# Optimization experiments

Measured on AMD Instinct MI355X. Metric: run time of the kernel, lower is better.

## Reference

```python
import jax, jax.numpy as jnp
import numpy as np

D = 1024   # input_dim
H = 16     # num_heads
DH = D // H  # attention_dim per head
B, S = 4, 2048


def setup_inputs() -> dict:
    key = jax.random.key(0)
    ks = jax.random.split(key, 12)
    sc = 1.0 / np.sqrt(D)
    x = jax.random.normal(ks[0], (B, S, D), dtype=jnp.float32)
    # per-head Q/K/V linears stacked: W [H, D, DH], b [H, DH]
    Wq = jax.random.normal(ks[1], (H, D, DH), dtype=jnp.float32) * sc
    bq = jax.random.normal(ks[2], (H, DH), dtype=jnp.float32) * 0.01
    Wk = jax.random.normal(ks[3], (H, D, DH), dtype=jnp.float32) * sc
    bk = jax.random.normal(ks[4], (H, DH), dtype=jnp.float32) * 0.01
    Wv = jax.random.normal(ks[5], (H, D, DH), dtype=jnp.float32) * sc
    bv = jax.random.normal(ks[6], (H, DH), dtype=jnp.float32) * 0.01
    Wo = jax.random.normal(ks[7], (D, D), dtype=jnp.float32) * sc
    bo = jax.random.normal(ks[8], (D,), dtype=jnp.float32) * 0.01
    ln_w = jnp.ones((D,), dtype=jnp.float32)
    ln_b = jnp.zeros((D,), dtype=jnp.float32)
    return {"x": x, "Wq": Wq, "bq": bq, "Wk": Wk, "bk": bk,
            "Wv": Wv, "bv": bv, "Wo": Wo, "bo": bo,
            "ln_w": ln_w, "ln_b": ln_b}


def _layer_norm(x, w, b, eps=1e-5):
    mu = jnp.mean(x, axis=-1, keepdims=True)
    var = jnp.var(x, axis=-1, keepdims=True)
    return (x - mu) * jax.lax.rsqrt(var + eps) * w + b


def reference(x, Wq, bq, Wk, bk, Wv, bv, Wo, bo, ln_w, ln_b):
    # batched per-head projections: [B,S,D] x [H,D,DH] -> [B,H,S,DH]
    q = jnp.einsum('bsd,hde->bhse', x, Wq) + bq[None, :, None, :]
    k = jnp.einsum('bsd,hde->bhse', x, Wk) + bk[None, :, None, :]
    v = jnp.einsum('bsd,hde->bhse', x, Wv) + bv[None, :, None, :]
    scores = jnp.einsum('bhse,bhte->bhst', q, k) / np.sqrt(DH).astype(np.float32)
    weights = jax.nn.softmax(scores, axis=-1)
    attn = jnp.einsum('bhst,bhte->bhse', weights, v)          # [B,H,S,DH]
    concat = attn.transpose(0, 2, 1, 3).reshape(B, S, D)       # head-major concat
    out = concat @ Wo + bo
    return _layer_norm(x + out, ln_w, ln_b)
```

## Files before the change

kernel.cpp:

```cpp
#include <hip/hip_runtime.h>
#include <hip/hip_bf16.h>
#include <stdint.h>

constexpr int D  = 1024;
constexpr int H  = 16;
constexpr int DH = 64;
constexpr int B  = 4;
constexpr int S  = 2048;
constexpr int BS = B * S;
constexpr int NQKV = 3 * D;

typedef __attribute__((ext_vector_type(8))) short bf16x8;
typedef __attribute__((ext_vector_type(4))) float f32x4;
typedef __attribute__((ext_vector_type(16))) float f32x16;
typedef __attribute__((ext_vector_type(4))) unsigned short us4;
typedef __attribute__((ext_vector_type(4))) unsigned int u32x4;
typedef unsigned short ushort_t;

using gu32 = __attribute__((address_space(1))) unsigned int;
using lu32 = __attribute__((address_space(3))) unsigned int;

__device__ __forceinline__ void gload_lds16(const void* g, void* l) {
  __builtin_amdgcn_global_load_lds((gu32*)g, (lu32*)l, 16, 0, 0);
}

__device__ __forceinline__ ushort_t f2bf(float f) {
  uint32_t u = __builtin_bit_cast(uint32_t, f);
  u += 0x7FFFu + ((u >> 16) & 1u);
  return (ushort_t)(u >> 16);
}

__device__ __forceinline__ unsigned cvtpk(float lo, float hi) {
  unsigned r;
  asm("v_cvt_pk_bf16_f32 %0, %1, %2" : "=v"(r) : "v"(lo), "v"(hi));
  return r;
}

__device__ __forceinline__ void xch4(unsigned& w0, unsigned& w1,
                                     unsigned& w2, unsigned& w3, int hi) {
  unsigned sx = hi ? w0 : w2;
  unsigned sy = hi ? w1 : w3;
  sx = (unsigned)__shfl_xor((int)sx, 32, 64);
  sy = (unsigned)__shfl_xor((int)sy, 32, 64);
  if (hi) { w0 = sx; w1 = sy; } else { w2 = sx; w3 = sy; }
}

__global__ __launch_bounds__(256) void k_conv_x(const float* __restrict__ x,
                                                ushort_t* __restrict__ xb) {
  int i = (blockIdx.x * 256 + threadIdx.x) * 4;
  float4 v = *(const float4*)(x + i);
  us4 o;
  o[0] = f2bf(v.x); o[1] = f2bf(v.y); o[2] = f2bf(v.z); o[3] = f2bf(v.w);
  *(us4*)(xb + i) = o;
}

__global__ __launch_bounds__(256) void k_conv_w(const float* __restrict__ Wq,
                                                const float* __restrict__ Wk,
                                                const float* __restrict__ Wv,
                                                ushort_t* __restrict__ wt) {
  __shared__ ushort_t tile[64][65];
  const int bid = blockIdx.x;
  const int which = bid >> 8;
  const int hh = (bid >> 4) & 15;
  const int d0 = (bid & 15) * 64;
  const float* src = (which == 0) ? Wq : (which == 1) ? Wk : Wv;
  const int t = threadIdx.x;
  const int dd = t >> 4, e4 = (t & 15) * 4;
#pragma unroll
  for (int p = 0; p < 4; ++p) {
    int d = dd + p * 16;
    float4 v = *(const float4*)(src + ((size_t)hh * D + d0 + d) * DH + e4);
    tile[e4 + 0][d] = f2bf(v.x);
    tile[e4 + 1][d] = f2bf(v.y);
    tile[e4 + 2][d] = f2bf(v.z);
    tile[e4 + 3][d] = f2bf(v.w);
  }
  __syncthreads();
  const int e = t >> 2, dp = (t & 3) * 16;
  ushort_t* dst = wt + (size_t)(which * 1024 + hh * 64 + e) * 1024 + d0 + dp;
  us4 o[4];
#pragma unroll
  for (int g = 0; g < 4; ++g)
#pragma unroll
    for (int j = 0; j < 4; ++j) o[g][j] = tile[e][dp + g * 4 + j];
#pragma unroll
  for (int g = 0; g < 4; ++g) *(us4*)(dst + g * 4) = o[g];
}

__global__ __launch_bounds__(256) void k_conv_wo(const float* __restrict__ Wo,
                                                 ushort_t* __restrict__ wot) {
  __shared__ ushort_t tile[64][65];
  const int bid = blockIdx.x;
  const int c0 = (bid >> 4) * 64;
  const int d0 = (bid & 15) * 64;
  const int t = threadIdx.x;
  const int dd = t >> 4, e4 = (t & 15) * 4;
#pragma unroll
  for (int p = 0; p < 4; ++p) {
    int d = dd + p * 16;
    float4 v = *(const float4*)(Wo + (size_t)(d0 + d) * 1024 + c0 + e4);
    tile[e4 + 0][d] = f2bf(v.x);
    tile[e4 + 1][d] = f2bf(v.y);
    tile[e4 + 2][d] = f2bf(v.z);
    tile[e4 + 3][d] = f2bf(v.w);
  }
  __syncthreads();
  const int e = t >> 2, dp = (t & 3) * 16;
  ushort_t* dst = wot + (size_t)(c0 + e) * 1024 + d0 + dp;
  us4 o[4];
#pragma unroll
  for (int g = 0; g < 4; ++g)
#pragma unroll
    for (int j = 0; j < 4; ++j) o[g][j] = tile[e][dp + g * 4 + j];
#pragma unroll
  for (int g = 0; g < 4; ++g) *(us4*)(dst + g * 4) = o[g];
}

__device__ __forceinline__ void gemm_core_256x128(const ushort_t* __restrict__ A,
                                                  const ushort_t* __restrict__ Bt,
                                                  int m0, int n0,
                                                  f32x4 acc[4][4], char* lds) {
  const int t = threadIdx.x;
  const int lane = t & 63, w = t >> 6;
  const int wm = w >> 1, wn = w & 1;
  const int lrow = lane & 15;
  const int chx = (((lane >> 4) ^ ((lrow >> 1) & 3)) << 4);

#pragma unroll
  for (int mi = 0; mi < 4; mi++)
#pragma unroll
    for (int ni = 0; ni < 4; ni++) acc[mi][ni] = f32x4{0.f, 0.f, 0.f, 0.f};

  const int prow = t >> 2;
  const int sw16 = (((t & 3) ^ ((prow >> 1) & 3)) << 4);
  const char* sA0 = (const char*)A  + (size_t)(m0 + prow) * 2048 + sw16;
  const char* sB0 = (const char*)Bt + (size_t)(n0 + prow) * 2048 + sw16;

  auto STAGE = [&](int kt) {
    char* bb = lds + (kt % 3) * 24576;
    const size_t ko = (size_t)kt * 64;
    gload_lds16(sA0 + ko,              bb + w * 1024);
    gload_lds16(sA0 + 128 * 2048 + ko, bb + 8192 + w * 1024);
    gload_lds16(sB0 + ko,              bb + 16384 + w * 1024);
  };

  STAGE(0); STAGE(1);

  for (int kt = 0; kt < 32; ++kt) {
    if (kt < 31) asm volatile("s_waitcnt vmcnt(3)" ::: "memory");
    else         asm volatile("s_waitcnt vmcnt(0)" ::: "memory");
    __builtin_amdgcn_sched_barrier(0);
    __builtin_amdgcn_s_barrier();
    __builtin_amdgcn_sched_barrier(0);
    if (kt + 2 < 32) STAGE(kt + 2);
    const char* bb = lds + (kt % 3) * 24576;
    const char* aB = bb + wm * 4096 + lrow * 64 + chx;
    const char* bB = bb + 16384 + wn * 4096 + lrow * 64 + chx;
    bf16x8 af[4], bf[4];
#pragma unroll
    for (int mi = 0; mi < 4; mi++) af[mi] = *(const bf16x8*)(aB + mi * 1024);
#pragma unroll
    for (int ni = 0; ni < 4; ni++) bf[ni] = *(const bf16x8*)(bB + ni * 1024);
    __builtin_amdgcn_s_setprio(1);
#pragma unroll
    for (int mi = 0; mi < 4; mi++)
#pragma unroll
      for (int ni = 0; ni < 4; ni++)
        acc[mi][ni] = __builtin_amdgcn_mfma_f32_16x16x32_bf16(af[mi], bf[ni], acc[mi][ni], 0, 0, 0);
    __builtin_amdgcn_s_setprio(0);
  }
}

__global__ __launch_bounds__(512, 2) void k_qkv_gemm(const ushort_t* __restrict__ xb,
                                                     const ushort_t* __restrict__ wt,
                                                     const float* __restrict__ bq,
                                                     const float* __restrict__ bk,
                                                     const float* __restrict__ bv,
                                                     ushort_t* __restrict__ q_ws,
                                                     ushort_t* __restrict__ k_ws,
                                                     ushort_t* __restrict__ vT_ws) {
  __shared__ __align__(16) char lds[3][24576];
  const int bid = blockIdx.x;
  const int wg = (bid & 7) * 96 + (bid >> 3);
  const int tm = wg / 24, tn = wg - tm * 24;
  const int m0 = tm * 256, n0 = tn * 128;
  f32x4 acc[4][4];
  gemm_core_256x128(xb, wt, m0, n0, acc, &lds[0][0]);

  constexpr float QSC = 0.18033688011112042f;
  const int t = threadIdx.x, lane = t & 63, w = t >> 6;
  const int wm = w >> 1, wn = w & 1;
  const int lrow = lane & 15, lgrp = lane >> 4;
#pragma unroll
  for (int mi = 0; mi < 4; mi++) {
    int rbase = m0 + wm * 64 + mi * 16 + lgrp * 4;
    int bb = rbase >> 11, ss0 = rbase & 2047;
#pragma unroll
    for (int ni = 0; ni < 4; ni++) {
      int c = n0 + wn * 64 + ni * 16 + lrow;
      int which = c >> 10, cl = c & 1023;
      int hh = cl >> 6, e = cl & 63;
      if (which == 0) {
        float bias = bq[cl];
#pragma unroll
        for (int i = 0; i < 4; i++)
          q_ws[((bb * H + hh) * S + ss0 + i) * 64 + e] = f2bf((acc[mi][ni][i] + bias) * QSC);
      } else if (which == 1) {
        float bias = bk[cl];
#pragma unroll
        for (int i = 0; i < 4; i++)
          k_ws[((bb * H + hh) * S + ss0 + i) * 64 + e] = f2bf(acc[mi][ni][i] + bias);
      } else {
        float bias = bv[cl];
        us4 pv;
#pragma unroll
        for (int i = 0; i < 4; i++) pv[i] = f2bf(acc[mi][ni][i] + bias);
        *(us4*)(vT_ws + (size_t)((bb * H + hh) * 64 + e) * S + ss0) = pv;
      }
    }
  }
}

__global__ __launch_bounds__(512, 2) void k_out_gemm(const ushort_t* __restrict__ attn_bf,
                                                     const ushort_t* __restrict__ wot,
                                                     const float* __restrict__ bo,
                                                     float* __restrict__ z) {
  __shared__ __align__(16) char lds[3][24576];
  const int bid = blockIdx.x;
  const int wg = (bid & 7) * 32 + (bid >> 3);
  const int tm = wg >> 3, tn = wg & 7;
  const int m0 = tm * 256, n0 = tn * 128;
  f32x4 acc[4][4];
  gemm_core_256x128(attn_bf, wot, m0, n0, acc, &lds[0][0]);

  const int t = threadIdx.x, lane = t & 63, w = t >> 6;
  const int wm = w >> 1, wn = w & 1;
  const int lrow = lane & 15, lgrp = lane >> 4;
#pragma unroll
  for (int mi = 0; mi < 4; mi++) {
    int rbase = m0 + wm * 64 + mi * 16 + lgrp * 4;
#pragma unroll
    for (int ni = 0; ni < 4; ni++) {
      int c = n0 + wn * 64 + ni * 16 + lrow;
#pragma unroll
      for (int i = 0; i < 4; i++)
        z[(size_t)(rbase + i) * D + c] = acc[mi][ni][i] + bo[c];
    }
  }
}

__global__ __launch_bounds__(512, 4) void k_attn(const ushort_t* __restrict__ q_ws,
                                                 const ushort_t* __restrict__ k_ws,
                                                 const ushort_t* __restrict__ vT_ws,
                                                 ushort_t* __restrict__ attn_bf) {
  __shared__ __align__(16) char lds[2][16384];
  const int bid = blockIdx.x;
  const int bh = ((bid & 7) << 3) | (bid >> 6);
  const int qt = (bid >> 3) & 7;
  const int bb = bh >> 4, hh = bh & 15;
  const char* qp = (const char*)(q_ws + (size_t)bh * S * 64);
  const char* kp = (const char*)(k_ws + (size_t)bh * S * 64);
  const char* vp = (const char*)(vT_ws + (size_t)bh * 64 * S);

  const int t = threadIdx.x, lane = t & 63, w = t >> 6;
  const int l31 = lane & 31, hi = lane >> 5;
  const int swz = (lane & 7) << 4;

  const int r0 = t >> 3;
  const int c0 = ((t & 7) << 4) ^ ((r0 & 7) << 4);

  const char* qrow = qp + (size_t)(qt * 256 + w * 32 + l31) * 128;
  bf16x8 qf[4];
#pragma unroll
  for (int w16 = 0; w16 < 4; ++w16)
    qf[w16] = *(const bf16x8*)(qrow + w16 * 32 + hi * 16);

  f32x16 oA, oB;
#pragma unroll
  for (int r = 0; r < 16; ++r) { oA[r] = 0.f; oB[r] = 0.f; }
  float m_run = -1e30f, l_run = 0.f;

  gload_lds16(kp + r0 * 128 + c0,  lds[0] + w * 1024 + (lane << 4));
  gload_lds16(vp + r0 * 4096 + c0, lds[0] + 8192 + w * 1024 + (lane << 4));
  __syncthreads();

  for (int tt = 0; tt < 32; ++tt) {
    const int cur = tt & 1;
    const char* Klds = lds[cur];
    const char* Vlds = lds[cur] + 8192;
    if (tt + 1 < 32) {
      char* dN = lds[cur ^ 1];
      const int nb = tt + 1;
      gload_lds16(kp + nb * 8192 + r0 * 128 + c0, dN + w * 1024 + (lane << 4));
      gload_lds16(vp + r0 * 4096 + nb * 128 + c0, dN + 8192 + w * 1024 + (lane << 4));
    }

    f32x16 sA, sB;
#pragma unroll
    for (int r = 0; r < 16; ++r) { sA[r] = 0.f; sB[r] = 0.f; }
    const char* kb = Klds + l31 * 128;
    __builtin_amdgcn_s_setprio(1);
#pragma unroll
    for (int w16 = 0; w16 < 4; ++w16) {
      const int col = w16 * 32 + hi * 16;
      bf16x8 k0 = *(const bf16x8*)(kb + (col ^ swz));
      bf16x8 k1 = *(const bf16x8*)(kb + 4096 + (col ^ swz));
      sA = __builtin_amdgcn_mfma_f32_32x32x16_bf16(k0, qf[w16], sA, 0, 0, 0);
      sB = __builtin_amdgcn_mfma_f32_32x32x16_bf16(k1, qf[w16], sB, 0, 0, 0);
    }
    __builtin_amdgcn_s_setprio(0);

    float mx = fmaxf(sA[0], sA[1]);
#pragma unroll
    for (int r = 2; r < 16; r += 2) mx = fmaxf(fmaxf(mx, sA[r]), sA[r + 1]);
#pragma unroll
    for (int r = 0; r < 16; r += 2) mx = fmaxf(fmaxf(mx, sB[r]), sB[r + 1]);
    mx = fmaxf(mx, __shfl_xor(mx, 32, 64));
    if (__any(mx > m_run + 11.5416f)) {
      float nm = fmaxf(m_run, mx);
      float corr = __builtin_amdgcn_exp2f(m_run - nm);
      l_run *= corr;
#pragma unroll
      for (int r = 0; r < 16; ++r) { oA[r] *= corr; oB[r] *= corr; }
      m_run = nm;
    }
    float rs = 0.f;
#pragma unroll
    for (int r = 0; r < 16; ++r) {
      sA[r] = __builtin_amdgcn_exp2f(sA[r] - m_run);
      sB[r] = __builtin_amdgcn_exp2f(sB[r] - m_run);
      rs += sA[r] + sB[r];
    }
    rs += __shfl_xor(rs, 32, 64);
    l_run += rs;

    unsigned pk0[8], pk1[8];
#pragma unroll
    for (int g = 0; g < 4; ++g) {
      pk0[2*g]   = cvtpk(sA[4*g],   sA[4*g+1]);
      pk0[2*g+1] = cvtpk(sA[4*g+2], sA[4*g+3]);
      pk1[2*g]   = cvtpk(sB[4*g],   sB[4*g+1]);
      pk1[2*g+1] = cvtpk(sB[4*g+2], sB[4*g+3]);
    }
    xch4(pk0[0], pk0[1], pk0[2], pk0[3], hi);
    xch4(pk0[4], pk0[5], pk0[6], pk0[7], hi);
    xch4(pk1[0], pk1[1], pk1[2], pk1[3], hi);
    xch4(pk1[4], pk1[5], pk1[6], pk1[7], hi);
    bf16x8 pf[4];
    pf[0] = __builtin_bit_cast(bf16x8, u32x4{pk0[0], pk0[1], pk0[2], pk0[3]});
    pf[1] = __builtin_bit_cast(bf16x8, u32x4{pk0[4], pk0[5], pk0[6], pk0[7]});
    pf[2] = __builtin_bit_cast(bf16x8, u32x4{pk1[0], pk1[1], pk1[2], pk1[3]});
    pf[3] = __builtin_bit_cast(bf16x8, u32x4{pk1[4], pk1[5], pk1[6], pk1[7]});

    const char* vb = Vlds + l31 * 128;
    __builtin_amdgcn_s_setprio(1);
#pragma unroll
    for (int ks = 0; ks < 4; ++ks) {
      const int colv = ks * 32 + hi * 16;
      bf16x8 v0 = *(const bf16x8*)(vb + (colv ^ swz));
      bf16x8 v1 = *(const bf16x8*)(vb + 4096 + (colv ^ swz));
      oA = __builtin_amdgcn_mfma_f32_32x32x16_bf16(v0, pf[ks], oA, 0, 0, 0);
      oB = __builtin_amdgcn_mfma_f32_32x32x16_bf16(v1, pf[ks], oB, 0, 0, 0);
    }
    __builtin_amdgcn_s_setprio(0);

    __syncthreads();
  }

  const float inv = 1.f / l_run;
  unsigned ok0[8], ok1[8];
#pragma unroll
  for (int g = 0; g < 4; ++g) {
    ok0[2*g]   = cvtpk(oA[4*g] * inv,   oA[4*g+1] * inv);
    ok0[2*g+1] = cvtpk(oA[4*g+2] * inv, oA[4*g+3] * inv);
    ok1[2*g]   = cvtpk(oB[4*g] * inv,   oB[4*g+1] * inv);
    ok1[2*g+1] = cvtpk(oB[4*g+2] * inv, oB[4*g+3] * inv);
  }
  xch4(ok0[0], ok0[1], ok0[2], ok0[3], hi);
  xch4(ok0[4], ok0[5], ok0[6], ok0[7], hi);
  xch4(ok1[0], ok1[1], ok1[2], ok1[3], hi);
  xch4(ok1[4], ok1[5], ok1[6], ok1[7], hi);

  const int grow = bb * S + qt * 256 + w * 32 + l31;
  ushort_t* orow = attn_bf + (size_t)grow * 1024 + hh * 64;
  *(u32x4*)(orow + 8 * hi)      = u32x4{ok0[0], ok0[1], ok0[2], ok0[3]};
  *(u32x4*)(orow + 16 + 8 * hi) = u32x4{ok0[4], ok0[5], ok0[6], ok0[7]};
  *(u32x4*)(orow + 32 + 8 * hi) = u32x4{ok1[0], ok1[1], ok1[2], ok1[3]};
  *(u32x4*)(orow + 48 + 8 * hi) = u32x4{ok1[4], ok1[5], ok1[6], ok1[7]};
}

__global__ __launch_bounds__(256) void k_ln(const float* __restrict__ z,
                                            const float* __restrict__ x,
                                            const float* __restrict__ lnw,
                                            const float* __restrict__ lnb,
                                            float* __restrict__ out) {
  const int r = blockIdx.x;
  const int t = threadIdx.x, lane = t & 63, w = t >> 6;
  float4 zv = ((const float4*)(z + r * D))[t];
  float4 xv = ((const float4*)(x + r * D))[t];
  float y[4] = {zv.x + xv.x, zv.y + xv.y, zv.z + xv.z, zv.w + xv.w};
  float sum = y[0] + y[1] + y[2] + y[3];
  float sq  = y[0]*y[0] + y[1]*y[1] + y[2]*y[2] + y[3]*y[3];
#pragma unroll
  for (int d = 1; d < 64; d <<= 1) { sum += __shfl_xor(sum, d, 64); sq += __shfl_xor(sq, d, 64); }
  __shared__ float ssum[4], ssq[4];
  if (lane == 0) { ssum[w] = sum; ssq[w] = sq; }
  __syncthreads();
  sum = ssum[0] + ssum[1] + ssum[2] + ssum[3];
  sq  = ssq[0] + ssq[1] + ssq[2] + ssq[3];
  float mean = sum * (1.f / D);
  float var  = sq * (1.f / D) - mean * mean;
  float rstd = rsqrtf(var + 1e-5f);
  float4 wv = ((const float4*)lnw)[t];
  float4 bv = ((const float4*)lnb)[t];
  float4 ov;
  ov.x = (y[0] - mean) * rstd * wv.x + bv.x;
  ov.y = (y[1] - mean) * rstd * wv.y + bv.y;
  ov.z = (y[2] - mean) * rstd * wv.z + bv.z;
  ov.w = (y[3] - mean) * rstd * wv.w + bv.w;
  ((float4*)(out + r * D))[t] = ov;
}

extern "C" void kernel_launch(void* const* d_in, const int* in_sizes, int n_in,
                              void* d_out, int out_size, void* d_ws, size_t ws_size,
                              hipStream_t stream) {
  const float* x   = (const float*)d_in[0];
  const float* Wq  = (const float*)d_in[1];
  const float* bq  = (const float*)d_in[2];
  const float* Wk  = (const float*)d_in[3];
  const float* bk  = (const float*)d_in[4];
  const float* Wv  = (const float*)d_in[5];
  const float* bv  = (const float*)d_in[6];
  const float* Wo  = (const float*)d_in[7];
  const float* bo  = (const float*)d_in[8];
  const float* lnw = (const float*)d_in[9];
  const float* lnb = (const float*)d_in[10];

  char* ws = (char*)d_ws;
  ushort_t* xb    = (ushort_t*)(ws + 0);
  ushort_t* q_ws  = (ushort_t*)(ws + 16777216);
  ushort_t* wt    = (ushort_t*)(ws + 33554432);
  ushort_t* wot   = (ushort_t*)(ws + 39845888);
  ushort_t* k_ws  = (ushort_t*)(ws + 41943040);
  ushort_t* vT_ws = (ushort_t*)(ws + 58720256);
  ushort_t* attn  = (ushort_t*)(ws + 75497472);
  float*    z     = (float*)(ws + 0);

  k_conv_x<<<8192, 256, 0, stream>>>(x, xb);
  k_conv_w<<<768, 256, 0, stream>>>(Wq, Wk, Wv, wt);
  k_conv_wo<<<256, 256, 0, stream>>>(Wo, wot);
  k_qkv_gemm<<<768, 512, 0, stream>>>(xb, wt, bq, bk, bv, q_ws, k_ws, vT_ws);
  k_attn<<<512, 512, 0, stream>>>(q_ws, k_ws, vT_ws, attn);
  k_out_gemm<<<256, 512, 0, stream>>>(attn, wot, bo, z);
  k_ln<<<BS, 256, 0, stream>>>(z, x, lnw, lnb, (float*)d_out);
}
```

Measured before the change: 293.7 us.

## Merge conversion kernels, fold residual into out-GEMM, double attention KV tile

Merges the three fp32-to-bf16 conversion kernels into one launch, cutting two kernel launches. Moves the residual add of x into the output GEMM epilogue, so the layernorm kernel no longer reads x. The attention kernel now stages two 64-key blocks per LDS buffer (64KB LDS total), which halves the number of barriers and prefetch rounds. The extra LDS could limit how many attention workgroups fit per CU, and the epilogue now does an extra strided load of x.

```diff
diff --git a/kernel.cpp b/kernel.cpp
--- a/kernel.cpp
+++ b/kernel.cpp
@@ -45,31 +45,49 @@
   if (hi) { w0 = sx; w1 = sy; } else { w2 = sx; w3 = sy; }
 }
 
-__global__ __launch_bounds__(256) void k_conv_x(const float* __restrict__ x,
-                                                ushort_t* __restrict__ xb) {
-  int i = (blockIdx.x * 256 + threadIdx.x) * 4;
-  float4 v = *(const float4*)(x + i);
-  us4 o;
-  o[0] = f2bf(v.x); o[1] = f2bf(v.y); o[2] = f2bf(v.z); o[3] = f2bf(v.w);
-  *(us4*)(xb + i) = o;
-}
-
-__global__ __launch_bounds__(256) void k_conv_w(const float* __restrict__ Wq,
-                                                const float* __restrict__ Wk,
-                                                const float* __restrict__ Wv,
-                                                ushort_t* __restrict__ wt) {
+__global__ __launch_bounds__(256) void k_conv_all(const float* __restrict__ x,
+                                                  const float* __restrict__ Wq,
+                                                  const float* __restrict__ Wk,
+                                                  const float* __restrict__ Wv,
+                                                  const float* __restrict__ Wo,
+                                                  ushort_t* __restrict__ xb,
+                                                  ushort_t* __restrict__ wt,
+                                                  ushort_t* __restrict__ wot) {
   __shared__ ushort_t tile[64][65];
   const int bid = blockIdx.x;
-  const int which = bid >> 8;
-  const int hh = (bid >> 4) & 15;
-  const int d0 = (bid & 15) * 64;
-  const float* src = (which == 0) ? Wq : (which == 1) ? Wk : Wv;
   const int t = threadIdx.x;
+  if (bid < 8192) {
+    int i = (bid * 256 + t) * 4;
+    float4 v = *(const float4*)(x + i);
+    us4 o;
+    o[0] = f2bf(v.x); o[1] = f2bf(v.y); o[2] = f2bf(v.z); o[3] = f2bf(v.w);
+    *(us4*)(xb + i) = o;
+    return;
+  }
+  const float* src;
+  ushort_t* dstbase;
+  int d0, rowbase;
+  if (bid < 8960) {
+    int b = bid - 8192;
+    int which = b >> 8, hh = (b >> 4) & 15;
+    d0 = (b & 15) * 64;
+    src = ((which == 0) ? Wq : (which == 1) ? Wk : Wv) + (size_t)hh * D * DH;
+    dstbase = wt;
+    rowbase = which * 1024 + hh * 64;
+  } else {
+    int b = bid - 8960;
+    int c0 = (b >> 4) * 64;
+    d0 = (b & 15) * 64;
+    src = Wo + c0;
+    dstbase = wot;
+    rowbase = c0;
+  }
+  const int rstride = (bid < 8960) ? DH : 1024;
   const int dd = t >> 4, e4 = (t & 15) * 4;
 #pragma unroll
   for (int p = 0; p < 4; ++p) {
     int d = dd + p * 16;
-    float4 v = *(const float4*)(src + ((size_t)hh * D + d0 + d) * DH + e4);
+    float4 v = *(const float4*)(src + (size_t)(d0 + d) * rstride + e4);
     tile[e4 + 0][d] = f2bf(v.x);
     tile[e4 + 1][d] = f2bf(v.y);
     tile[e4 + 2][d] = f2bf(v.z);
@@ -77,36 +95,7 @@
   }
   __syncthreads();
   const int e = t >> 2, dp = (t & 3) * 16;
-  ushort_t* dst = wt + (size_t)(which * 1024 + hh * 64 + e) * 1024 + d0 + dp;
-  us4 o[4];
-#pragma unroll
-  for (int g = 0; g < 4; ++g)
-#pragma unroll
-    for (int j = 0; j < 4; ++j) o[g][j] = tile[e][dp + g * 4 + j];
-#pragma unroll
-  for (int g = 0; g < 4; ++g) *(us4*)(dst + g * 4) = o[g];
-}
-
-__global__ __launch_bounds__(256) void k_conv_wo(const float* __restrict__ Wo,
-                                                 ushort_t* __restrict__ wot) {
-  __shared__ ushort_t tile[64][65];
-  const int bid = blockIdx.x;
-  const int c0 = (bid >> 4) * 64;
-  const int d0 = (bid & 15) * 64;
-  const int t = threadIdx.x;
-  const int dd = t >> 4, e4 = (t & 15) * 4;
-#pragma unroll
-  for (int p = 0; p < 4; ++p) {
-    int d = dd + p * 16;
-    float4 v = *(const float4*)(Wo + (size_t)(d0 + d) * 1024 + c0 + e4);
-    tile[e4 + 0][d] = f2bf(v.x);
-    tile[e4 + 1][d] = f2bf(v.y);
-    tile[e4 + 2][d] = f2bf(v.z);
-    tile[e4 + 3][d] = f2bf(v.w);
-  }
-  __syncthreads();
-  const int e = t >> 2, dp = (t & 3) * 16;
-  ushort_t* dst = wot + (size_t)(c0 + e) * 1024 + d0 + dp;
+  ushort_t* dst = dstbase + (size_t)(rowbase + e) * 1024 + d0 + dp;
   us4 o[4];
 #pragma unroll
   for (int g = 0; g < 4; ++g)
@@ -224,6 +213,7 @@
 __global__ __launch_bounds__(512, 2) void k_out_gemm(const ushort_t* __restrict__ attn_bf,
                                                      const ushort_t* __restrict__ wot,
                                                      const float* __restrict__ bo,
+                                                     const float* __restrict__ xres,
                                                      float* __restrict__ z) {
   __shared__ __align__(16) char lds[3][24576];
   const int bid = blockIdx.x;
@@ -243,8 +233,10 @@
     for (int ni = 0; ni < 4; ni++) {
       int c = n0 + wn * 64 + ni * 16 + lrow;
 #pragma unroll
-      for (int i = 0; i < 4; i++)
-        z[(size_t)(rbase + i) * D + c] = acc[mi][ni][i] + bo[c];
+      for (int i = 0; i < 4; i++) {
+        size_t idx = (size_t)(rbase + i) * D + c;
+        z[idx] = acc[mi][ni][i] + bo[c] + xres[idx];
+      }
     }
   }
 }
@@ -253,7 +245,7 @@
                                                  const ushort_t* __restrict__ k_ws,
                                                  const ushort_t* __restrict__ vT_ws,
                                                  ushort_t* __restrict__ attn_bf) {
-  __shared__ __align__(16) char lds[2][16384];
+  __shared__ __align__(16) char lds[2][32768];
   const int bid = blockIdx.x;
   const int bh = ((bid & 7) << 3) | (bid >> 6);
   const int qt = (bid >> 3) & 7;
@@ -268,6 +260,7 @@
 
   const int r0 = t >> 3;
   const int c0 = ((t & 7) << 4) ^ ((r0 & 7) << 4);
+  const int dst16 = t << 4;
 
   const char* qrow = qp + (size_t)(qt * 256 + w * 32 + l31) * 128;
   bf16x8 qf[4];
@@ -280,89 +273,99 @@
   for (int r = 0; r < 16; ++r) { oA[r] = 0.f; oB[r] = 0.f; }
   float m_run = -1e30f, l_run = 0.f;
 
-  gload_lds16(kp + r0 * 128 + c0,  lds[0] + w * 1024 + (lane << 4));
-  gload_lds16(vp + r0 * 4096 + c0, lds[0] + 8192 + w * 1024 + (lane << 4));
+#pragma unroll
+  for (int j = 0; j < 2; ++j) {
+    gload_lds16(kp + j * 8192 + r0 * 128 + c0,  lds[0] + j * 8192 + dst16);
+    gload_lds16(vp + r0 * 4096 + j * 128 + c0,  lds[0] + 16384 + j * 8192 + dst16);
+  }
   __syncthreads();
 
-  for (int tt = 0; tt < 32; ++tt) {
-    const int cur = tt & 1;
-    const char* Klds = lds[cur];
-    const char* Vlds = lds[cur] + 8192;
-    if (tt + 1 < 32) {
+  for (int ph = 0; ph < 16; ++ph) {
+    const int cur = ph & 1;
+    if (ph + 1 < 16) {
       char* dN = lds[cur ^ 1];
-      const int nb = tt + 1;
-      gload_lds16(kp + nb * 8192 + r0 * 128 + c0, dN + w * 1024 + (lane << 4));
-      gload_lds16(vp + r0 * 4096 + nb * 128 + c0, dN + 8192 + w * 1024 + (lane << 4));
+      const int nb0 = (ph + 1) * 2;
+#pragma unroll
+      for (int j = 0; j < 2; ++j) {
+        gload_lds16(kp + (size_t)(nb0 + j) * 8192 + r0 * 128 + c0, dN + j * 8192 + dst16);
+        gload_lds16(vp + r0 * 4096 + (nb0 + j) * 128 + c0, dN + 16384 + j * 8192 + dst16);
+      }
     }
 
-    f32x16 sA, sB;
-#pragma unroll
-    for (int r = 0; r < 16; ++r) { sA[r] = 0.f; sB[r] = 0.f; }
-    const char* kb = Klds + l31 * 128;
-    __builtin_amdgcn_s_setprio(1);
-#pragma unroll
-    for (int w16 = 0; w16 < 4; ++w16) {
-      const int col = w16 * 32 + hi * 16;
-      bf16x8 k0 = *(const bf16x8*)(kb + (col ^ swz));
-      bf16x8 k1 = *(const bf16x8*)(kb + 4096 + (col ^ swz));
-      sA = __builtin_amdgcn_mfma_f32_32x32x16_bf16(k0, qf[w16], sA, 0, 0, 0);
-      sB = __builtin_amdgcn_mfma_f32_32x32x16_bf16(k1, qf[w16], sB, 0, 0, 0);
+#pragma unroll
+    for (int sub = 0; sub < 2; ++sub) {
+      const char* Klds = lds[cur] + sub * 8192;
+      const char* Vlds = lds[cur] + 16384 + sub * 8192;
+
+      f32x16 sA, sB;
+#pragma unroll
+      for (int r = 0; r < 16; ++r) { sA[r] = 0.f; sB[r] = 0.f; }
+      const char* kb = Klds + l31 * 128;
+      __builtin_amdgcn_s_setprio(1);
+#pragma unroll
+      for (int w16 = 0; w16 < 4; ++w16) {
+        const int col = w16 * 32 + hi * 16;
+        bf16x8 k0 = *(const bf16x8*)(kb + (col ^ swz));
+        bf16x8 k1 = *(const bf16x8*)(kb + 4096 + (col ^ swz));
+        sA = __builtin_amdgcn_mfma_f32_32x32x16_bf16(k0, qf[w16], sA, 0, 0, 0);
+        sB = __builtin_amdgcn_mfma_f32_32x32x16_bf16(k1, qf[w16], sB, 0, 0, 0);
+      }
+      __builtin_amdgcn_s_setprio(0);
+
+      float mx = fmaxf(sA[0], sA[1]);
+#pragma unroll
+      for (int r = 2; r < 16; r += 2) mx = fmaxf(fmaxf(mx, sA[r]), sA[r + 1]);
+#pragma unroll
+      for (int r = 0; r < 16; r += 2) mx = fmaxf(fmaxf(mx, sB[r]), sB[r + 1]);
+      mx = fmaxf(mx, __shfl_xor(mx, 32, 64));
+      if (__any(mx > m_run + 11.5416f)) {
+        float nm = fmaxf(m_run, mx);
+        float corr = __builtin_amdgcn_exp2f(m_run - nm);
+        l_run *= corr;
+#pragma unroll
+        for (int r = 0; r < 16; ++r) { oA[r] *= corr; oB[r] *= corr; }
+        m_run = nm;
+      }
+      float rs = 0.f;
+#pragma unroll
+      for (int r = 0; r < 16; ++r) {
+        sA[r] = __builtin_amdgcn_exp2f(sA[r] - m_run);
+        sB[r] = __builtin_amdgcn_exp2f(sB[r] - m_run);
+        rs += sA[r] + sB[r];
+      }
+      rs += __shfl_xor(rs, 32, 64);
+      l_run += rs;
+
+      unsigned pk0[8], pk1[8];
+#pragma unroll
+      for (int g = 0; g < 4; ++g) {
+        pk0[2*g]   = cvtpk(sA[4*g],   sA[4*g+1]);
+        pk0[2*g+1] = cvtpk(sA[4*g+2], sA[4*g+3]);
+        pk1[2*g]   = cvtpk(sB[4*g],   sB[4*g+1]);
+        pk1[2*g+1] = cvtpk(sB[4*g+2], sB[4*g+3]);
+      }
+      xch4(pk0[0], pk0[1], pk0[2], pk0[3], hi);
+      xch4(pk0[4], pk0[5], pk0[6], pk0[7], hi);
+      xch4(pk1[0], pk1[1], pk1[2], pk1[3], hi);
+      xch4(pk1[4], pk1[5], pk1[6], pk1[7], hi);
+      bf16x8 pf[4];
+      pf[0] = __builtin_bit_cast(bf16x8, u32x4{pk0[0], pk0[1], pk0[2], pk0[3]});
+      pf[1] = __builtin_bit_cast(bf16x8, u32x4{pk0[4], pk0[5], pk0[6], pk0[7]});
+      pf[2] = __builtin_bit_cast(bf16x8, u32x4{pk1[0], pk1[1], pk1[2], pk1[3]});
+      pf[3] = __builtin_bit_cast(bf16x8, u32x4{pk1[4], pk1[5], pk1[6], pk1[7]});
+
+      const char* vb = Vlds + l31 * 128;
+      __builtin_amdgcn_s_setprio(1);
+#pragma unroll
+      for (int ks = 0; ks < 4; ++ks) {
+        const int colv = ks * 32 + hi * 16;
+        bf16x8 v0 = *(const bf16x8*)(vb + (colv ^ swz));
+        bf16x8 v1 = *(const bf16x8*)(vb + 4096 + (colv ^ swz));
+        oA = __builtin_amdgcn_mfma_f32_32x32x16_bf16(v0, pf[ks], oA, 0, 0, 0);
+        oB = __builtin_amdgcn_mfma_f32_32x32x16_bf16(v1, pf[ks], oB, 0, 0, 0);
+      }
+      __builtin_amdgcn_s_setprio(0);
     }
-    __builtin_amdgcn_s_setprio(0);
-
-    float mx = fmaxf(sA[0], sA[1]);
-#pragma unroll
-    for (int r = 2; r < 16; r += 2) mx = fmaxf(fmaxf(mx, sA[r]), sA[r + 1]);
-#pragma unroll
-    for (int r = 0; r < 16; r += 2) mx = fmaxf(fmaxf(mx, sB[r]), sB[r + 1]);
-    mx = fmaxf(mx, __shfl_xor(mx, 32, 64));
-    if (__any(mx > m_run + 11.5416f)) {
-      float nm = fmaxf(m_run, mx);
-      float corr = __builtin_amdgcn_exp2f(m_run - nm);
-      l_run *= corr;
-#pragma unroll
-      for (int r = 0; r < 16; ++r) { oA[r] *= corr; oB[r] *= corr; }
-      m_run = nm;
-    }
-    float rs = 0.f;
-#pragma unroll
-    for (int r = 0; r < 16; ++r) {
-      sA[r] = __builtin_amdgcn_exp2f(sA[r] - m_run);
-      sB[r] = __builtin_amdgcn_exp2f(sB[r] - m_run);
-      rs += sA[r] + sB[r];
-    }
-    rs += __shfl_xor(rs, 32, 64);
-    l_run += rs;
-
-    unsigned pk0[8], pk1[8];
-#pragma unroll
-    for (int g = 0; g < 4; ++g) {
-      pk0[2*g]   = cvtpk(sA[4*g],   sA[4*g+1]);
-      pk0[2*g+1] = cvtpk(sA[4*g+2], sA[4*g+3]);
-      pk1[2*g]   = cvtpk(sB[4*g],   sB[4*g+1]);
-      pk1[2*g+1] = cvtpk(sB[4*g+2], sB[4*g+3]);
-    }
-    xch4(pk0[0], pk0[1], pk0[2], pk0[3], hi);
-    xch4(pk0[4], pk0[5], pk0[6], pk0[7], hi);
-    xch4(pk1[0], pk1[1], pk1[2], pk1[3], hi);
-    xch4(pk1[4], pk1[5], pk1[6], pk1[7], hi);
-    bf16x8 pf[4];
-    pf[0] = __builtin_bit_cast(bf16x8, u32x4{pk0[0], pk0[1], pk0[2], pk0[3]});
-    pf[1] = __builtin_bit_cast(bf16x8, u32x4{pk0[4], pk0[5], pk0[6], pk0[7]});
-    pf[2] = __builtin_bit_cast(bf16x8, u32x4{pk1[0], pk1[1], pk1[2], pk1[3]});
-    pf[3] = __builtin_bit_cast(bf16x8, u32x4{pk1[4], pk1[5], pk1[6], pk1[7]});
-
-    const char* vb = Vlds + l31 * 128;
-    __builtin_amdgcn_s_setprio(1);
-#pragma unroll
-    for (int ks = 0; ks < 4; ++ks) {
-      const int colv = ks * 32 + hi * 16;
-      bf16x8 v0 = *(const bf16x8*)(vb + (colv ^ swz));
-      bf16x8 v1 = *(const bf16x8*)(vb + 4096 + (colv ^ swz));
-      oA = __builtin_amdgcn_mfma_f32_32x32x16_bf16(v0, pf[ks], oA, 0, 0, 0);
-      oB = __builtin_amdgcn_mfma_f32_32x32x16_bf16(v1, pf[ks], oB, 0, 0, 0);
-    }
-    __builtin_amdgcn_s_setprio(0);
 
     __syncthreads();
   }
@@ -390,15 +393,13 @@
 }
 
 __global__ __launch_bounds__(256) void k_ln(const float* __restrict__ z,
-                                            const float* __restrict__ x,
                                             const float* __restrict__ lnw,
                                             const float* __restrict__ lnb,
                                             float* __restrict__ out) {
   const int r = blockIdx.x;
   const int t = threadIdx.x, lane = t & 63, w = t >> 6;
   float4 zv = ((const float4*)(z + r * D))[t];
-  float4 xv = ((const float4*)(x + r * D))[t];
-  float y[4] = {zv.x + xv.x, zv.y + xv.y, zv.z + xv.z, zv.w + xv.w};
+  float y[4] = {zv.x, zv.y, zv.z, zv.w};
   float sum = y[0] + y[1] + y[2] + y[3];
   float sq  = y[0]*y[0] + y[1]*y[1] + y[2]*y[2] + y[3]*y[3];
 #pragma unroll
@@ -446,11 +447,9 @@
   ushort_t* attn  = (ushort_t*)(ws + 75497472);
   float*    z     = (float*)(ws + 0);
 
-  k_conv_x<<<8192, 256, 0, stream>>>(x, xb);
-  k_conv_w<<<768, 256, 0, stream>>>(Wq, Wk, Wv, wt);
-  k_conv_wo<<<256, 256, 0, stream>>>(Wo, wot);
+  k_conv_all<<<9216, 256, 0, stream>>>(x, Wq, Wk, Wv, Wo, xb, wt, wot);
   k_qkv_gemm<<<768, 512, 0, stream>>>(xb, wt, bq, bk, bv, q_ws, k_ws, vT_ws);
   k_attn<<<512, 512, 0, stream>>>(q_ws, k_ws, vT_ws, attn);
-  k_out_gemm<<<256, 512, 0, stream>>>(attn, wot, bo, z);
-  k_ln<<<BS, 256, 0, stream>>>(z, x, lnw, lnb, (float*)d_out);
-}
+  k_out_gemm<<<256, 512, 0, stream>>>(attn, wot, bo, x, z);
+  k_ln<<<BS, 256, 0, stream>>>(z, lnw, lnb, (float*)d_out);
+}
```

After: 288.5 us. Within noise of the previous version (-1.8%).
